# Kernel tuning notes

Measured on AMD Instinct MI355X. Metric: run time of the kernel, lower is better.

## Reference

```python
import jax, jax.numpy as jnp
import numpy as np

# VTM 'standard' luma taps: 16 phases x 8 taps, log2Norm=12, numFracShift=4, numFracMask=15
LUMA_TAPS = np.array([
    [0, 0, 0, 64, 0, 0, 0, 0], [0, 1, -3, 63, 4, -2, 1, 0], [-1, 2, -5, 62, 8, -3, 1, 0],
    [-1, 3, -8, 60, 13, -4, 1, 0], [-1, 4, -10, 58, 17, -5, 1, 0], [-1, 4, -11, 52, 26, -8, 3, -1],
    [-1, 3, -9, 47, 31, -10, 4, -1], [-1, 4, -11, 45, 34, -10, 4, -1], [-1, 4, -11, 40, 40, -11, 4, -1],
    [-1, 4, -10, 34, 45, -11, 4, -1], [-1, 4, -10, 31, 47, -9, 3, -1], [-1, 3, -8, 26, 52, -11, 4, -1],
    [0, 1, -5, 17, 58, -10, 4, -1], [0, 1, -4, 13, 60, -8, 3, -1], [0, 1, -3, 8, 62, -5, 2, -1],
    [0, 1, -2, 4, 63, -3, 1, 0]], dtype=np.float32)

FILTER_LEN = 8
NUM_FRAC_SHIFT = 4
NUM_FRAC_MASK = 15
LOG2_NORM = 12


def _phase_tables(n_out, scale, in_size):
    """Static (numpy) per-output-index gather indices [n_out, L] and phase ids [n_out]."""
    center = FILTER_LEN // 2 - 1
    ref_fixed = (np.arange(n_out, dtype=np.int64) * (1 << 14) / scale).astype(np.int64)
    ref_phase = ref_fixed >> (14 - NUM_FRAC_SHIFT)
    integer = ref_phase >> NUM_FRAC_SHIFT
    frac = (ref_phase & NUM_FRAC_MASK).astype(np.int32)
    k = np.arange(FILTER_LEN, dtype=np.int64)
    idx = np.clip(integer[:, None] + k[None, :] - center, 0, in_size - 1).astype(np.int32)
    return idx, frac


def setup_inputs() -> dict:
    key = jax.random.key(0)
    x = jax.random.normal(key, (4, 3, 540, 960), dtype=jnp.float32)
    taps = jnp.asarray(LUMA_TAPS)  # [16, 8] fixed buffer
    return {"x": x, "taps": taps, "scale": 2}


def reference(x, taps, scale):
    B, C, H, W = x.shape
    newW = int(round(W * scale))
    newH = int(round(H * scale))

    # --- horizontal pass: [B,C,H,W] -> [B,C,H,newW]
    idx_w, frac_w = _phase_tables(newW, scale, W)      # [newW,L], [newW]
    wts_w = taps[frac_w]                                # [newW, L]
    buf = jnp.zeros((B, C, H, newW), dtype=jnp.float32)
    for k in range(FILTER_LEN):
        buf = buf + wts_w[:, k] * x[..., idx_w[:, k]]   # broadcast over last dim

    # --- vertical pass: [B,C,H,newW] -> [B,C,newH,newW]
    idx_h, frac_h = _phase_tables(newH, scale, H)
    wts_h = taps[frac_h]                                # [newH, L]
    acc = jnp.zeros((B, C, newH, newW), dtype=jnp.float32)
    for k in range(FILTER_LEN):
        acc = acc + wts_h[:, k][None, None, :, None] * buf[:, :, idx_h[:, k], :]

    rnd = jnp.float32(1 << (LOG2_NORM - 1))
    return (acc + rnd) / jnp.float32(1 << LOG2_NORM)
```

## Files before the change

kernel.cpp:

```cpp
#include <hip/hip_runtime.h>

namespace {

constexpr int Wd = 960;
constexpr int Hd = 540;
constexpr int NW = 1920;
constexpr int NH = 1080;
constexpr int BC = 12;

constexpr int TW = 64;
constexpr int TH = 16;
constexpr int XR = TH + 7;
constexpr int XC = TW + 7;
constexpr int XCP = 72;
constexpr int NT = 256;

__global__ __launch_bounds__(NT)
void vtm_up2_kernel(const float* __restrict__ x, float* __restrict__ out) {
    __shared__ float xs[XR][XCP];
    __shared__ float hs[XR][TW];

    const int tid = threadIdx.x;
    const int c0  = blockIdx.x * TW;
    const int r0  = blockIdx.y * TH;
    const int bc  = blockIdx.z;

    const float* __restrict__ xin = x   + (size_t)bc * (Hd * Wd);
    float*       __restrict__ op  = out + (size_t)bc * (NH * NW);

    for (int i = tid; i < XR * XCP; i += NT) {
        int lr = i / XCP;
        int lc = i - lr * XCP;
        int lcc = lc >= XC ? XC - 1 : lc;
        int gr = r0 + lr - 3;
        gr = gr < 0 ? 0 : (gr > Hd - 1 ? Hd - 1 : gr);
        int gc = c0 + lcc - 3;
        gc = gc < 0 ? 0 : (gc > Wd - 1 ? Wd - 1 : gc);
        xs[lr][lc] = xin[gr * Wd + gc];
    }
    __syncthreads();

    const float T0 = -1.0f, T1 = 4.0f, T2 = -11.0f, T3 = 40.0f;

    for (int i = tid; i < XR * TW; i += NT) {
        int lr = i >> 6;
        int c  = i & 63;
        float s = T0 * (xs[lr][c]     + xs[lr][c + 7])
                + T1 * (xs[lr][c + 1] + xs[lr][c + 6])
                + T2 * (xs[lr][c + 2] + xs[lr][c + 5])
                + T3 * (xs[lr][c + 3] + xs[lr][c + 4]);
        hs[lr][c] = s;
    }
    __syncthreads();

    const int qc  = tid & 63;
    const int qr0 = tid >> 6;

#pragma unroll
    for (int p = 0; p < 4; ++p) {
        const int qr = qr0 + 4 * p;
        const int orow = r0 + qr;
        if (orow >= Hd) continue;

        const float a = xs[qr + 3][qc + 3];
        const float h = hs[qr + 3][qc];

        const float v = T0 * (xs[qr][qc + 3]     + xs[qr + 7][qc + 3])
                      + T1 * (xs[qr + 1][qc + 3] + xs[qr + 6][qc + 3])
                      + T2 * (xs[qr + 2][qc + 3] + xs[qr + 5][qc + 3])
                      + T3 * (xs[qr + 3][qc + 3] + xs[qr + 4][qc + 3]);

        const float hv = T0 * (hs[qr][qc]     + hs[qr + 7][qc])
                       + T1 * (hs[qr + 1][qc] + hs[qr + 6][qc])
                       + T2 * (hs[qr + 2][qc] + hs[qr + 5][qc])
                       + T3 * (hs[qr + 3][qc] + hs[qr + 4][qc]);

        float2 even, odd;
        even.x = a + 0.5f;
        even.y = h * (1.0f / 64.0f) + 0.5f;
        odd.x  = v * (1.0f / 64.0f) + 0.5f;
        odd.y  = hv * (1.0f / 4096.0f) + 0.5f;

        float* p0 = op + (size_t)(2 * orow) * NW + 2 * (c0 + qc);
        *reinterpret_cast<float2*>(p0)      = even;
        *reinterpret_cast<float2*>(p0 + NW) = odd;
    }
}

}

extern "C" void kernel_launch(void* const* d_in, const int* in_sizes, int n_in,
                              void* d_out, int out_size, void* d_ws, size_t ws_size,
                              hipStream_t stream) {
    const float* x = (const float*)d_in[0];
    float* out = (float*)d_out;

    dim3 grid(Wd / TW , (Hd + TH - 1) / TH , BC );
    vtm_up2_kernel<<<grid, NT, 0, stream>>>(x, out);
}
```

Before: 131.3 us.

## Vectorize tile loads, filter passes and output stores with float4

Interior blocks now load the input tile with aligned float4 global reads; only edge blocks keep the scalar clamped path. The tile is shifted by 4 columns for 16-byte alignment. Each thread now computes four adjacent columns of one output row, using float4 shared-memory reads and writes. This replaces the scalar per-column loop with 16-byte output stores. It lowers instruction count and improves store width, but adds a branch between load paths and reduces per-thread parallelism in the final stage.

```diff
diff --git a/kernel.cpp b/kernel.cpp
--- a/kernel.cpp
+++ b/kernel.cpp
@@ -11,80 +11,113 @@
 constexpr int TW = 64;
 constexpr int TH = 16;
 constexpr int XR = TH + 7;
-constexpr int XC = TW + 7;
-constexpr int XCP = 72;
+constexpr int GEP = 72;
 constexpr int NT = 256;
 
 __global__ __launch_bounds__(NT)
 void vtm_up2_kernel(const float* __restrict__ x, float* __restrict__ out) {
-    __shared__ float xs[XR][XCP];
-    __shared__ float hs[XR][TW];
+    __shared__ float ge[XR][GEP];
+    __shared__ float go[XR][TW];
 
     const int tid = threadIdx.x;
-    const int c0  = blockIdx.x * TW;
+    const int bx  = blockIdx.x;
+    const int c0  = bx * TW;
     const int r0  = blockIdx.y * TH;
     const int bc  = blockIdx.z;
 
     const float* __restrict__ xin = x   + (size_t)bc * (Hd * Wd);
     float*       __restrict__ op  = out + (size_t)bc * (NH * NW);
 
-    for (int i = tid; i < XR * XCP; i += NT) {
-        int lr = i / XCP;
-        int lc = i - lr * XCP;
-        int lcc = lc >= XC ? XC - 1 : lc;
-        int gr = r0 + lr - 3;
-        gr = gr < 0 ? 0 : (gr > Hd - 1 ? Hd - 1 : gr);
-        int gc = c0 + lcc - 3;
-        gc = gc < 0 ? 0 : (gc > Wd - 1 ? Wd - 1 : gc);
-        xs[lr][lc] = xin[gr * Wd + gc];
+    if (bx >= 1 && bx <= 13) {
+        for (int i = tid; i < XR * 18; i += NT) {
+            int r = i / 18, q = i - r * 18;
+            int gr = r0 + r - 3; gr = gr < 0 ? 0 : (gr > Hd - 1 ? Hd - 1 : gr);
+            float4 v = *reinterpret_cast<const float4*>(xin + gr * Wd + (c0 - 4) + 4 * q);
+            *reinterpret_cast<float4*>(&ge[r][4 * q]) = v;
+        }
+    } else {
+        for (int i = tid; i < XR * GEP; i += NT) {
+            int r = i / GEP, q = i - r * GEP;
+            int gr = r0 + r - 3; gr = gr < 0 ? 0 : (gr > Hd - 1 ? Hd - 1 : gr);
+            int gc = c0 - 4 + q; gc = gc < 0 ? 0 : (gc > Wd - 1 ? Wd - 1 : gc);
+            ge[r][q] = xin[gr * Wd + gc];
+        }
     }
     __syncthreads();
 
     const float T0 = -1.0f, T1 = 4.0f, T2 = -11.0f, T3 = 40.0f;
 
-    for (int i = tid; i < XR * TW; i += NT) {
-        int lr = i >> 6;
-        int c  = i & 63;
-        float s = T0 * (xs[lr][c]     + xs[lr][c + 7])
-                + T1 * (xs[lr][c + 1] + xs[lr][c + 6])
-                + T2 * (xs[lr][c + 2] + xs[lr][c + 5])
-                + T3 * (xs[lr][c + 3] + xs[lr][c + 4]);
-        hs[lr][c] = s;
+    for (int t = tid; t < XR * 16; t += NT) {
+        int r = t >> 4, g = t & 15;
+        float4 a = *reinterpret_cast<const float4*>(&ge[r][4 * g]);
+        float4 b = *reinterpret_cast<const float4*>(&ge[r][4 * g + 4]);
+        float4 c = *reinterpret_cast<const float4*>(&ge[r][4 * g + 8]);
+        float w0 = a.x, w1 = a.y, w2 = a.z, w3 = a.w;
+        float w4 = b.x, w5 = b.y, w6 = b.z, w7 = b.w;
+        float w8 = c.x, w9 = c.y, w10 = c.z, w11 = c.w;
+        float4 h;
+        h.x = T0 * (w1 + w8)  + T1 * (w2 + w7)  + T2 * (w3 + w6)  + T3 * (w4 + w5);
+        h.y = T0 * (w2 + w9)  + T1 * (w3 + w8)  + T2 * (w4 + w7)  + T3 * (w5 + w6);
+        h.z = T0 * (w3 + w10) + T1 * (w4 + w9)  + T2 * (w5 + w8)  + T3 * (w6 + w7);
+        h.w = T0 * (w4 + w11) + T1 * (w5 + w10) + T2 * (w6 + w9)  + T3 * (w7 + w8);
+        *reinterpret_cast<float4*>(&go[r][4 * g]) = h;
     }
     __syncthreads();
 
-    const int qc  = tid & 63;
-    const int qr0 = tid >> 6;
+    const int cg = tid & 15;
+    const int qr = tid >> 4;
+    const int orow = r0 + qr;
+    if (orow >= Hd) return;
 
-#pragma unroll
-    for (int p = 0; p < 4; ++p) {
-        const int qr = qr0 + 4 * p;
-        const int orow = r0 + qr;
-        if (orow >= Hd) continue;
+    const float4 e0 = *reinterpret_cast<const float4*>(&ge[qr + 3][4 * cg + 4]);
+    const float4 h0 = *reinterpret_cast<const float4*>(&go[qr + 3][4 * cg]);
 
-        const float a = xs[qr + 3][qc + 3];
-        const float h = hs[qr + 3][qc];
+    float4 ve, vh;
+    {
+        const float4 a0 = *reinterpret_cast<const float4*>(&ge[qr + 0][4 * cg + 4]);
+        const float4 a7 = *reinterpret_cast<const float4*>(&ge[qr + 7][4 * cg + 4]);
+        const float4 a1 = *reinterpret_cast<const float4*>(&ge[qr + 1][4 * cg + 4]);
+        const float4 a6 = *reinterpret_cast<const float4*>(&ge[qr + 6][4 * cg + 4]);
+        const float4 a2 = *reinterpret_cast<const float4*>(&ge[qr + 2][4 * cg + 4]);
+        const float4 a5 = *reinterpret_cast<const float4*>(&ge[qr + 5][4 * cg + 4]);
+        const float4 a3 = *reinterpret_cast<const float4*>(&ge[qr + 3][4 * cg + 4]);
+        const float4 a4 = *reinterpret_cast<const float4*>(&ge[qr + 4][4 * cg + 4]);
+        ve.x = T0 * (a0.x + a7.x) + T1 * (a1.x + a6.x) + T2 * (a2.x + a5.x) + T3 * (a3.x + a4.x);
+        ve.y = T0 * (a0.y + a7.y) + T1 * (a1.y + a6.y) + T2 * (a2.y + a5.y) + T3 * (a3.y + a4.y);
+        ve.z = T0 * (a0.z + a7.z) + T1 * (a1.z + a6.z) + T2 * (a2.z + a5.z) + T3 * (a3.z + a4.z);
+        ve.w = T0 * (a0.w + a7.w) + T1 * (a1.w + a6.w) + T2 * (a2.w + a5.w) + T3 * (a3.w + a4.w);
+    }
+    {
+        const float4 b0 = *reinterpret_cast<const float4*>(&go[qr + 0][4 * cg]);
+        const float4 b7 = *reinterpret_cast<const float4*>(&go[qr + 7][4 * cg]);
+        const float4 b1 = *reinterpret_cast<const float4*>(&go[qr + 1][4 * cg]);
+        const float4 b6 = *reinterpret_cast<const float4*>(&go[qr + 6][4 * cg]);
+        const float4 b2 = *reinterpret_cast<const float4*>(&go[qr + 2][4 * cg]);
+        const float4 b5 = *reinterpret_cast<const float4*>(&go[qr + 5][4 * cg]);
+        const float4 b3 = *reinterpret_cast<const float4*>(&go[qr + 3][4 * cg]);
+        const float4 b4 = *reinterpret_cast<const float4*>(&go[qr + 4][4 * cg]);
+        vh.x = T0 * (b0.x + b7.x) + T1 * (b1.x + b6.x) + T2 * (b2.x + b5.x) + T3 * (b3.x + b4.x);
+        vh.y = T0 * (b0.y + b7.y) + T1 * (b1.y + b6.y) + T2 * (b2.y + b5.y) + T3 * (b3.y + b4.y);
+        vh.z = T0 * (b0.z + b7.z) + T1 * (b1.z + b6.z) + T2 * (b2.z + b5.z) + T3 * (b3.z + b4.z);
+        vh.w = T0 * (b0.w + b7.w) + T1 * (b1.w + b6.w) + T2 * (b2.w + b5.w) + T3 * (b3.w + b4.w);
+    }
 
-        const float v = T0 * (xs[qr][qc + 3]     + xs[qr + 7][qc + 3])
-                      + T1 * (xs[qr + 1][qc + 3] + xs[qr + 6][qc + 3])
-                      + T2 * (xs[qr + 2][qc + 3] + xs[qr + 5][qc + 3])
-                      + T3 * (xs[qr + 3][qc + 3] + xs[qr + 4][qc + 3]);
+    const float i64 = 1.0f / 64.0f, i4096 = 1.0f / 4096.0f;
+    float4 evA, evB, odA, odB;
+    evA.x = e0.x + 0.5f;        evA.y = h0.x * i64 + 0.5f;
+    evA.z = e0.y + 0.5f;        evA.w = h0.y * i64 + 0.5f;
+    evB.x = e0.z + 0.5f;        evB.y = h0.z * i64 + 0.5f;
+    evB.z = e0.w + 0.5f;        evB.w = h0.w * i64 + 0.5f;
+    odA.x = ve.x * i64 + 0.5f;  odA.y = vh.x * i4096 + 0.5f;
+    odA.z = ve.y * i64 + 0.5f;  odA.w = vh.y * i4096 + 0.5f;
+    odB.x = ve.z * i64 + 0.5f;  odB.y = vh.z * i4096 + 0.5f;
+    odB.z = ve.w * i64 + 0.5f;  odB.w = vh.w * i4096 + 0.5f;
 
-        const float hv = T0 * (hs[qr][qc]     + hs[qr + 7][qc])
-                       + T1 * (hs[qr + 1][qc] + hs[qr + 6][qc])
-                       + T2 * (hs[qr + 2][qc] + hs[qr + 5][qc])
-                       + T3 * (hs[qr + 3][qc] + hs[qr + 4][qc]);
-
-        float2 even, odd;
-        even.x = a + 0.5f;
-        even.y = h * (1.0f / 64.0f) + 0.5f;
-        odd.x  = v * (1.0f / 64.0f) + 0.5f;
-        odd.y  = hv * (1.0f / 4096.0f) + 0.5f;
-
-        float* p0 = op + (size_t)(2 * orow) * NW + 2 * (c0 + qc);
-        *reinterpret_cast<float2*>(p0)      = even;
-        *reinterpret_cast<float2*>(p0 + NW) = odd;
-    }
+    float* p0 = op + (size_t)(2 * orow) * NW + 2 * c0 + 8 * cg;
+    *reinterpret_cast<float4*>(p0)          = evA;
+    *reinterpret_cast<float4*>(p0 + 4)      = evB;
+    *reinterpret_cast<float4*>(p0 + NW)     = odA;
+    *reinterpret_cast<float4*>(p0 + NW + 4) = odB;
 }
 
 }
```

Measured after the change: 131.8 us. About the same (+0.4%).
